# Performance work log

Hardware: AMD Instinct MI355X
Metric: run time of the kernel (lower is better)

The kernel has to match this reference:

```python
import jax, jax.numpy as jnp
import numpy as np

EPS_AGG = 1e-6  # torch code adds 1e-6 to scatter weight sums
EPS_BN = 1e-5


def _pix_idx(loc_orig, H, W):
    # map normalized coords in [-1,1] to flat pixel index on an HxW grid
    loc = jnp.clip(loc_orig, -1.0, 1.0) * 0.5 + 0.5
    ix = jnp.round(loc[..., 0] * (W - 1)).astype(jnp.int32)
    iy = jnp.round(loc[..., 1] * (H - 1)).astype(jnp.int32)
    return iy * W + ix  # [B, N0]


def token2map(x, loc_orig, idx_agg, H, W):
    # scatter token features to a dense map, averaging collisions
    B, N, C = x.shape
    N0 = idx_agg.shape[1]
    idx_hw = _pix_idx(loc_orig, H, W)                                   # [B, N0]
    tok = jnp.take_along_axis(x, idx_agg[..., None], axis=1)            # [B, N0, C]
    flat = (idx_hw + jnp.arange(B, dtype=jnp.int32)[:, None] * (H * W)).reshape(-1)
    sums = jax.ops.segment_sum(tok.reshape(-1, C), flat, num_segments=B * H * W)
    cnt = jax.ops.segment_sum(jnp.ones((B * N0,), x.dtype), flat, num_segments=B * H * W)
    out = sums / (cnt[:, None] + EPS_AGG)
    return out.reshape(B, H, W, C).transpose(0, 3, 1, 2)                # [B, C, H, W]


def map2token(fmap, Nt, loc_orig, idx_agg_t, agg_weight_t):
    # gather map pixels back to Nt target tokens, weighted-averaging per token
    B, C, H, W = fmap.shape
    idx_hw = _pix_idx(loc_orig, H, W)                                   # [B, N0]
    pix = fmap.transpose(0, 2, 3, 1).reshape(B, H * W, C)
    gath = jnp.take_along_axis(pix, idx_hw[..., None], axis=1)          # [B, N0, C]
    flat = (idx_agg_t + jnp.arange(B, dtype=jnp.int32)[:, None] * Nt).reshape(-1)
    num = jax.ops.segment_sum((gath * agg_weight_t[..., None]).reshape(-1, C), flat, num_segments=B * Nt)
    den = jax.ops.segment_sum(agg_weight_t.reshape(-1), flat, num_segments=B * Nt)
    return (num / (den[:, None] + EPS_AGG)).reshape(B, Nt, C)


def token_downup(x, idx_agg_s, idx_agg_t, agg_weight_t, Nt):
    # weighted aggregation from N source tokens to Nt target tokens via N0 original positions
    B, N, C = x.shape
    src = jnp.take_along_axis(x, idx_agg_s[..., None], axis=1)          # [B, N0, C]
    flat = (idx_agg_t + jnp.arange(B, dtype=jnp.int32)[:, None] * Nt).reshape(-1)
    num = jax.ops.segment_sum((src * agg_weight_t[..., None]).reshape(-1, C), flat, num_segments=B * Nt)
    den = jax.ops.segment_sum(agg_weight_t.reshape(-1), flat, num_segments=B * Nt)
    return (num / (den[:, None] + EPS_AGG)).reshape(B, Nt, C)


def batchnorm(x, gamma, beta):
    # BatchNorm2d on [B,C,Nt,1] == per-channel stats over (B, Nt); x here is [B, Nt, C]
    mu = x.mean(axis=(0, 1), keepdims=True)
    var = x.var(axis=(0, 1), keepdims=True)
    return (x - mu) * jax.lax.rsqrt(var + EPS_BN) * gamma + beta


def setup_inputs() -> dict:
    key = jax.random.key(0)
    ks = jax.random.split(key, 12)
    B, N, N0, Nt, Cin, Cout, H, W = 32, 1568, 3136, 784, 256, 512, 56, 56
    x = jax.random.normal(ks[0], (B, N, Cin), dtype=jnp.float32)
    loc_orig = jax.random.uniform(ks[1], (B, N0, 2), dtype=jnp.float32, minval=-1.0, maxval=1.0)
    idx_agg = jax.random.randint(ks[2], (B, N0), 0, N, dtype=jnp.int32)
    agg_weight = jax.random.uniform(ks[3], (B, N0), dtype=jnp.float32)
    idx_agg_t = jax.random.randint(ks[4], (B, N0), 0, Nt, dtype=jnp.int32)
    agg_weight_t = jax.random.uniform(ks[5], (B, N0), dtype=jnp.float32)
    dw_w = jax.random.normal(ks[6], (Cin, 1, 3, 3), dtype=jnp.float32) * 0.1     # depthwise 3x3
    skip_w = jax.random.normal(ks[7], (Cin,), dtype=jnp.float32) * 0.1           # depthwise 1x1
    conv_w = jax.random.normal(ks[8], (Cout, Cin), dtype=jnp.float32) * (1.0 / np.sqrt(Cin))
    gamma1 = jnp.ones((Cin,), jnp.float32); beta1 = jnp.zeros((Cin,), jnp.float32)
    gamma2 = jnp.ones((Cout,), jnp.float32); beta2 = jnp.zeros((Cout,), jnp.float32)
    return {"x": x, "loc_orig": loc_orig, "idx_agg": idx_agg, "agg_weight": agg_weight,
            "idx_agg_t": idx_agg_t, "agg_weight_t": agg_weight_t, "H": H, "W": W, "Nt": Nt,
            "dw_w": dw_w, "skip_w": skip_w, "conv_w": conv_w,
            "gamma1": gamma1, "beta1": beta1, "gamma2": gamma2, "beta2": beta2}


def reference(x, loc_orig, idx_agg, agg_weight, idx_agg_t, agg_weight_t, H, W, Nt,
              dw_w, skip_w, conv_w, gamma1, beta1, gamma2, beta2):
    # token -> map scatter
    x_map = token2map(x, loc_orig, idx_agg, H, W)                       # [B, Cin, H, W]
    # 3x3 depthwise conv, stride 2, padding 1
    Cin = x_map.shape[1]
    x_map = jax.lax.conv_general_dilated(
        x_map, dw_w, window_strides=(2, 2), padding=((1, 1), (1, 1)),
        feature_group_count=Cin, dimension_numbers=("NCHW", "OIHW", "NCHW"))    # [B, Cin, H/2, W/2]
    # map -> target tokens gather
    x_back = map2token(x_map, Nt, loc_orig, idx_agg_t, agg_weight_t)    # [B, Nt, Cin]
    # skip path: token downsample + 1x1 depthwise (per-channel scale)
    xs = token_downup(x, idx_agg, idx_agg_t, agg_weight_t, Nt)          # [B, Nt, Cin]
    xs = xs * skip_w                                                    # dw_skip, groups=Cin, k=1
    y = xs + x_back
    y = batchnorm(y, gamma1, beta1)
    y = jnp.einsum("bnc,oc->bno", y, conv_w)                            # 1x1 conv Cin->Cout
    y = batchnorm(y, gamma2, beta2)
    return jax.nn.relu(y)                                               # [B, Nt, Cout]
```

## Files before the change

kernel.cpp:

```cpp
#include <hip/hip_runtime.h>

constexpr int B    = 32;
constexpr int N    = 1568;
constexpr int N0   = 3136;
constexpr int Nt   = 784;
constexpr int Cin  = 256;
constexpr int Cout = 512;
constexpr int H    = 56;
constexpr int W    = 56;
constexpr int HW   = 3136;
constexpr int Ho   = 28;
constexpr int Wo   = 28;
constexpr int HWo  = 784;
constexpr int RR   = B * Nt;
constexpr int NE   = B * N0;
constexpr int NBP  = B * HW;
constexpr int NBT  = B * Nt;
constexpr int NBO  = B * HWo;
constexpr int SB   = NBT + NBO;
constexpr int NCHUNK = SB / 256;
constexpr int NG   = 32;

constexpr size_t W_HISTP = 0;
constexpr size_t W_HISTS = NBP;
constexpr size_t W_S2SUM = NBP + SB;
constexpr size_t W_S2SQ  = W_S2SUM + Cout;
constexpr size_t W_S1P   = W_S2SQ + Cout;
constexpr size_t W_S1QP  = W_S1P + (size_t)NG * Cin;
constexpr size_t W_MEND  = W_S1QP + (size_t)NG * Cin;
constexpr size_t W_OFF   = W_MEND;
constexpr size_t W_CUR   = W_OFF + SB + 8;
constexpr size_t W_PC    = W_CUR + SB;
constexpr size_t W_BSUM  = W_PC + NE;
constexpr size_t W_LT    = W_BSUM + 512;
constexpr size_t W_LC    = W_LT + (size_t)2 * NE;
constexpr size_t W_CONVB = W_LC + (size_t)8 * NE;
constexpr size_t W_YBF   = W_CONVB + (size_t)B * HWo * Cin / 2;
constexpr size_t W_WFB   = W_YBF + (size_t)RR * Cin / 2;
constexpr size_t W_BIAS  = W_WFB + (size_t)Cout * Cin / 2;
constexpr size_t W_ZB    = W_BIAS + Cout;

__device__ __forceinline__ int pix_of(float t, float scale) {
    t = fminf(fmaxf(t, -1.0f), 1.0f);
    float u = __fadd_rn(__fmul_rn(t, 0.5f), 0.5f);
    return (int)rintf(__fmul_rn(u, scale));
}
__device__ __forceinline__ unsigned short f2bf(float f) {
    unsigned int u = __float_as_uint(f);
    u = (u + 0x7fffu + ((u >> 16) & 1u)) >> 16;
    return (unsigned short)u;
}
__device__ __forceinline__ float bf2f(unsigned short h) {
    return __uint_as_float(((unsigned int)h) << 16);
}
__device__ __forceinline__ void gload_lds16(const void* g, void* lds) {
    __builtin_amdgcn_global_load_lds(
        (const __attribute__((address_space(1))) void*)g,
        (__attribute__((address_space(3))) void*)lds, 16, 0, 0);
}

__global__ void k_hist(const float* __restrict__ loc, const int* __restrict__ idxt,
                       int* __restrict__ histP, int* __restrict__ histS,
                       int* __restrict__ pc) {
    int i = blockIdx.x * 256 + threadIdx.x;
    if (i >= NE) return;
    int b = i / N0;
    float lx = loc[(size_t)2 * i], ly = loc[(size_t)2 * i + 1];
    int ix = pix_of(lx, 55.0f), iy = pix_of(ly, 55.0f);
    int jx = pix_of(lx, 27.0f), jy = pix_of(ly, 27.0f);
    int p56 = iy * W + ix, p28 = jy * Wo + jx;
    pc[i] = p56 | (p28 << 16);
    atomicAdd(&histP[b * HW + p56], 1);
    atomicAdd(&histS[b * Nt + idxt[i]], 1);
    int oy_lo = iy >> 1, oy_hi = min(Ho - 1, (iy + 1) >> 1);
    int ox_lo = ix >> 1, ox_hi = min(Wo - 1, (ix + 1) >> 1);
    for (int oy = oy_lo; oy <= oy_hi; ++oy)
        for (int ox = ox_lo; ox <= ox_hi; ++ox)
            atomicAdd(&histS[NBT + b * HWo + oy * Wo + ox], 1);
}

__global__ void k_scanA(const int* __restrict__ hist, int* __restrict__ bsum) {
    __shared__ int sm[256];
    int i = blockIdx.x * 256 + threadIdx.x;
    sm[threadIdx.x] = hist[i];
    __syncthreads();
    for (int d = 128; d > 0; d >>= 1) {
        if (threadIdx.x < d) sm[threadIdx.x] += sm[threadIdx.x + d];
        __syncthreads();
    }
    if (threadIdx.x == 0) bsum[blockIdx.x] = sm[0];
}

__global__ void k_scanC(const int* __restrict__ hist, const int* __restrict__ bsum,
                        int* __restrict__ off, int* __restrict__ cur) {
    __shared__ int sm[256];
    __shared__ int sb[256];
    int t = threadIdx.x;
    int i = blockIdx.x * 256 + t;
    sb[t] = (t < NCHUNK && t < (int)blockIdx.x) ? bsum[t] : 0;
    int v = hist[i];
    sm[t] = v; __syncthreads();
    for (int d = 128; d > 0; d >>= 1) {
        if (t < d) sb[t] += sb[t + d];
        __syncthreads();
    }
    int base = sb[0];
    __syncthreads();
    for (int d = 1; d < 256; d <<= 1) {
        int u = (t >= d) ? sm[t - d] : 0;
        __syncthreads();
        sm[t] += u;
        __syncthreads();
    }
    int excl = base + sm[t] - v;
    off[i] = excl; cur[i] = excl;
    if (i == SB - 1) off[SB] = excl + v;
}

__global__ void k_scat(const int* __restrict__ pc, const int* __restrict__ idxa,
                       const int* __restrict__ idxt, const float* __restrict__ wt,
                       const int* __restrict__ histP, int* __restrict__ cur,
                       int2* __restrict__ listT, int2* __restrict__ listC) {
    int i = blockIdx.x * 256 + threadIdx.x;
    if (i >= NE) return;
    int b = i / N0;
    int v = pc[i];
    int p56 = v & 0xFFFF, p28 = v >> 16;
    int s = idxa[i];
    int posT = atomicAdd(&cur[b * Nt + idxt[i]], 1);
    listT[posT] = make_int2(s | (p28 << 16), __float_as_int(wt[i]));
    float wrc = 1.0f / ((float)histP[b * HW + p56] + 1e-6f);
    int wrci = __float_as_int(wrc);
    int iy = p56 / W, ix = p56 - iy * W;
    int oy_lo = iy >> 1, oy_hi = min(Ho - 1, (iy + 1) >> 1);
    int ox_lo = ix >> 1, ox_hi = min(Wo - 1, (ix + 1) >> 1);
    for (int oy = oy_lo; oy <= oy_hi; ++oy)
        for (int ox = ox_lo; ox <= ox_hi; ++ox) {
            int tap = (iy - (2 * oy - 1)) * 3 + (ix - (2 * ox - 1));
            int posC = atomicAdd(&cur[NBT + b * HWo + oy * Wo + ox], 1) - NE;
            listC[posC] = make_int2(s | (tap << 16), wrci);
        }
}

__global__ __launch_bounds__(256) void k_gconv(const float* __restrict__ x,
        const int* __restrict__ off, const int2* __restrict__ listC,
        const float* __restrict__ dww, unsigned short* __restrict__ convb) {
    __shared__ float wsm[9 * 256];
    int t = threadIdx.x;
#pragma unroll
    for (int k = 0; k < 9; ++k) wsm[k * 256 + t] = dww[t * 9 + k];
    int wv = t >> 6, lane = t & 63;
    int blk = blockIdx.x * 4 + wv;
    int b   = __builtin_amdgcn_readfirstlane(blk / HWo);
    int st  = __builtin_amdgcn_readfirstlane(off[NBT + blk]) - NE;
    int en  = __builtin_amdgcn_readfirstlane(off[NBT + blk + 1]) - NE;
    __syncthreads();
    const float* xb = x + (size_t)b * N * Cin;
    float4 acc = make_float4(0.f, 0.f, 0.f, 0.f);
    for (int base = st; base < en; base += 64) {
        int n = en - base; if (n > 64) n = 64;
        int2 e = make_int2(0, 0);
        if (lane < n) e = listC[base + lane];
        int j = 0;
        for (; j + 4 <= n; j += 4) {
            int ex0 = __builtin_amdgcn_readlane(e.x, j + 0);
            int ey0 = __builtin_amdgcn_readlane(e.y, j + 0);
            int ex1 = __builtin_amdgcn_readlane(e.x, j + 1);
            int ey1 = __builtin_amdgcn_readlane(e.y, j + 1);
            int ex2 = __builtin_amdgcn_readlane(e.x, j + 2);
            int ey2 = __builtin_amdgcn_readlane(e.y, j + 2);
            int ex3 = __builtin_amdgcn_readlane(e.x, j + 3);
            int ey3 = __builtin_amdgcn_readlane(e.y, j + 3);
            float4 v0 = ((const float4*)(xb + (size_t)(ex0 & 0xFFFF) * Cin))[lane];
            float4 v1 = ((const float4*)(xb + (size_t)(ex1 & 0xFFFF) * Cin))[lane];
            float4 v2 = ((const float4*)(xb + (size_t)(ex2 & 0xFFFF) * Cin))[lane];
            float4 v3 = ((const float4*)(xb + (size_t)(ex3 & 0xFFFF) * Cin))[lane];
            float4 w0 = *(const float4*)&wsm[(ex0 >> 16) * 256 + lane * 4];
            float4 w1 = *(const float4*)&wsm[(ex1 >> 16) * 256 + lane * 4];
            float4 w2 = *(const float4*)&wsm[(ex2 >> 16) * 256 + lane * 4];
            float4 w3 = *(const float4*)&wsm[(ex3 >> 16) * 256 + lane * 4];
            float r0 = __int_as_float(ey0), r1 = __int_as_float(ey1);
            float r2 = __int_as_float(ey2), r3 = __int_as_float(ey3);
            acc.x = fmaf(v0.x * r0, w0.x, acc.x);
            acc.y = fmaf(v0.y * r0, w0.y, acc.y);
            acc.z = fmaf(v0.z * r0, w0.z, acc.z);
            acc.w = fmaf(v0.w * r0, w0.w, acc.w);
            acc.x = fmaf(v1.x * r1, w1.x, acc.x);
            acc.y = fmaf(v1.y * r1, w1.y, acc.y);
            acc.z = fmaf(v1.z * r1, w1.z, acc.z);
            acc.w = fmaf(v1.w * r1, w1.w, acc.w);
            acc.x = fmaf(v2.x * r2, w2.x, acc.x);
            acc.y = fmaf(v2.y * r2, w2.y, acc.y);
            acc.z = fmaf(v2.z * r2, w2.z, acc.z);
            acc.w = fmaf(v2.w * r2, w2.w, acc.w);
            acc.x = fmaf(v3.x * r3, w3.x, acc.x);
            acc.y = fmaf(v3.y * r3, w3.y, acc.y);
            acc.z = fmaf(v3.z * r3, w3.z, acc.z);
            acc.w = fmaf(v3.w * r3, w3.w, acc.w);
        }
        for (; j < n; ++j) {
            int ex = __builtin_amdgcn_readlane(e.x, j);
            int ey = __builtin_amdgcn_readlane(e.y, j);
            float4 v = ((const float4*)(xb + (size_t)(ex & 0xFFFF) * Cin))[lane];
            float4 wq = *(const float4*)&wsm[(ex >> 16) * 256 + lane * 4];
            float r = __int_as_float(ey);
            acc.x = fmaf(v.x * r, wq.x, acc.x);
            acc.y = fmaf(v.y * r, wq.y, acc.y);
            acc.z = fmaf(v.z * r, wq.z, acc.z);
            acc.w = fmaf(v.w * r, wq.w, acc.w);
        }
    }
    uint2 o;
    o.x = (unsigned int)f2bf(acc.x) | ((unsigned int)f2bf(acc.y) << 16);
    o.y = (unsigned int)f2bf(acc.z) | ((unsigned int)f2bf(acc.w) << 16);
    ((uint2*)(convb + (size_t)blk * Cin))[lane] = o;
}

__global__ __launch_bounds__(256) void k_gtok(const float* __restrict__ x,
        const unsigned short* __restrict__ convb, const int* __restrict__ off,
        const int2* __restrict__ listT, const float* __restrict__ skipw,
        unsigned short* __restrict__ ybf, float* __restrict__ s1p,
        float* __restrict__ s1qp) {
    __shared__ float smS[4][256];
    __shared__ float smQ[4][256];
    int t = threadIdx.x, wv = t >> 6, lane = t & 63;
    int bt = blockIdx.x * 4 + wv;
    int b  = __builtin_amdgcn_readfirstlane(bt / Nt);
    int st = __builtin_amdgcn_readfirstlane(off[bt]);
    int en = __builtin_amdgcn_readfirstlane(off[bt + 1]);
    const float* xb = x + (size_t)b * N * Cin;
    const unsigned short* cbb = convb + (size_t)b * HWo * Cin;
    float4 sk = ((const float4*)skipw)[lane];
    float4 acc = make_float4(0.f, 0.f, 0.f, 0.f);
    float wsum = 0.0f;
    for (int base = st; base < en; base += 64) {
        int n = en - base; if (n > 64) n = 64;
        int2 e = make_int2(0, 0);
        if (lane < n) e = listT[base + lane];
        int j = 0;
        for (; j + 2 <= n; j += 2) {
            int ex0 = __builtin_amdgcn_readlane(e.x, j + 0);
            int ey0 = __builtin_amdgcn_readlane(e.y, j + 0);
            int ex1 = __builtin_amdgcn_readlane(e.x, j + 1);
            int ey1 = __builtin_amdgcn_readlane(e.y, j + 1);
            float4 xv0 = ((const float4*)(xb + (size_t)(ex0 & 0xFFFF) * Cin))[lane];
            float4 xv1 = ((const float4*)(xb + (size_t)(ex1 & 0xFFFF) * Cin))[lane];
            uint2 cv0 = ((const uint2*)(cbb + (size_t)(ex0 >> 16) * Cin))[lane];
            uint2 cv1 = ((const uint2*)(cbb + (size_t)(ex1 >> 16) * Cin))[lane];
            float w0 = __int_as_float(ey0), w1 = __int_as_float(ey1);
            wsum += w0 + w1;
            acc.x = fmaf(w0, bf2f((unsigned short)(cv0.x & 0xffffu)) + sk.x * xv0.x, acc.x);
            acc.y = fmaf(w0, bf2f((unsigned short)(cv0.x >> 16))     + sk.y * xv0.y, acc.y);
            acc.z = fmaf(w0, bf2f((unsigned short)(cv0.y & 0xffffu)) + sk.z * xv0.z, acc.z);
            acc.w = fmaf(w0, bf2f((unsigned short)(cv0.y >> 16))     + sk.w * xv0.w, acc.w);
            acc.x = fmaf(w1, bf2f((unsigned short)(cv1.x & 0xffffu)) + sk.x * xv1.x, acc.x);
            acc.y = fmaf(w1, bf2f((unsigned short)(cv1.x >> 16))     + sk.y * xv1.y, acc.y);
            acc.z = fmaf(w1, bf2f((unsigned short)(cv1.y & 0xffffu)) + sk.z * xv1.z, acc.z);
            acc.w = fmaf(w1, bf2f((unsigned short)(cv1.y >> 16))     + sk.w * xv1.w, acc.w);
        }
        for (; j < n; ++j) {
            int ex = __builtin_amdgcn_readlane(e.x, j);
            int ey = __builtin_amdgcn_readlane(e.y, j);
            float4 xv = ((const float4*)(xb + (size_t)(ex & 0xFFFF) * Cin))[lane];
            uint2 cv = ((const uint2*)(cbb + (size_t)(ex >> 16) * Cin))[lane];
            float w = __int_as_float(ey);
            wsum += w;
            acc.x = fmaf(w, bf2f((unsigned short)(cv.x & 0xffffu)) + sk.x * xv.x, acc.x);
            acc.y = fmaf(w, bf2f((unsigned short)(cv.x >> 16))     + sk.y * xv.y, acc.y);
            acc.z = fmaf(w, bf2f((unsigned short)(cv.y & 0xffffu)) + sk.z * xv.z, acc.z);
            acc.w = fmaf(w, bf2f((unsigned short)(cv.y >> 16))     + sk.w * xv.w, acc.w);
        }
    }
    float rw = 1.0f / (wsum + 1e-6f);
    float y0 = acc.x * rw, y1 = acc.y * rw, y2 = acc.z * rw, y3 = acc.w * rw;
    smS[wv][lane * 4 + 0] = y0; smQ[wv][lane * 4 + 0] = y0 * y0;
    smS[wv][lane * 4 + 1] = y1; smQ[wv][lane * 4 + 1] = y1 * y1;
    smS[wv][lane * 4 + 2] = y2; smQ[wv][lane * 4 + 2] = y2 * y2;
    smS[wv][lane * 4 + 3] = y3; smQ[wv][lane * 4 + 3] = y3 * y3;
    uint2 o;
    o.x = (unsigned int)f2bf(y0) | ((unsigned int)f2bf(y1) << 16);
    o.y = (unsigned int)f2bf(y2) | ((unsigned int)f2bf(y3) << 16);
    ((uint2*)(ybf + (size_t)bt * Cin))[lane] = o;
    __syncthreads();
    float ps = smS[0][t] + smS[1][t] + smS[2][t] + smS[3][t];
    float pq = smQ[0][t] + smQ[1][t] + smQ[2][t] + smQ[3][t];
    int g = (blockIdx.x & (NG - 1)) * Cin + t;
    atomicAdd(&s1p[g],  ps);
    atomicAdd(&s1qp[g], pq);
}

__global__ void k_fold(const float* __restrict__ s1p, const float* __restrict__ s1qp,
                       const float* __restrict__ g1, const float* __restrict__ b1,
                       const float* __restrict__ convw, unsigned short* __restrict__ wfb,
                       float* __restrict__ bias) {
    int o = blockIdx.x, c = threadIdx.x;
    const float inv = 1.0f / (float)RR;
    float s = 0.0f, q = 0.0f;
#pragma unroll
    for (int g = 0; g < NG; ++g) { s += s1p[g * Cin + c]; q += s1qp[g * Cin + c]; }
    float mu  = s * inv;
    float var = q * inv - mu * mu;
    float a   = g1[c] / sqrtf(var + 1e-5f);
    float bs  = b1[c] - mu * a;
    float wv  = convw[(size_t)o * Cin + c];
    wfb[(size_t)o * Cin + c] = f2bf(wv * a);
    __shared__ float red[256];
    red[c] = wv * bs;
    __syncthreads();
    for (int st = 128; st > 0; st >>= 1) {
        if (c < st) red[c] += red[c + st];
        __syncthreads();
    }
    if (c == 0) bias[o] = red[0];
}

typedef __attribute__((ext_vector_type(8))) short short8;
typedef __attribute__((ext_vector_type(4))) float f32x4;

__global__ __launch_bounds__(256, 4) void k_gemm(const unsigned short* __restrict__ A,
        const unsigned short* __restrict__ Bt, const float* __restrict__ bias,
        unsigned short* __restrict__ zb, float* __restrict__ s2, float* __restrict__ s2q) {
    __shared__ unsigned short As[2][128 * 32];
    __shared__ unsigned short Bs[2][128 * 32];
    __shared__ float rsum[128], rsq[128];
    int m0 = blockIdx.x * 128, n0 = blockIdx.y * 128;
    int t = threadIdx.x;
    int wave = t >> 6, lane = t & 63;
    int wm = wave >> 1, wn = wave & 1;
    int l16 = lane & 15, lq = lane >> 4;
    if (t < 128) { rsum[t] = 0.0f; rsq[t] = 0.0f; }

    int r_off = lane >> 2;
    int sc    = (lane & 3) ^ ((lane >> 4) & 3);
    const unsigned short* Asrc = A  + (size_t)(m0 + r_off) * Cin + sc * 8;
    const unsigned short* Bsrc = Bt + (size_t)(n0 + r_off) * Cin + sc * 8;
    int r0a = wave * 32, r0b = r0a + 16;

    auto STAGE = [&](int buf, int k0) {
        gload_lds16(Asrc + (size_t)r0a * Cin + k0, &As[buf][r0a * 32]);
        gload_lds16(Asrc + (size_t)r0b * Cin + k0, &As[buf][r0b * 32]);
        gload_lds16(Bsrc + (size_t)r0a * Cin + k0, &Bs[buf][r0a * 32]);
        gload_lds16(Bsrc + (size_t)r0b * Cin + k0, &Bs[buf][r0b * 32]);
    };

    int ckoff = (lq ^ ((l16 >> 2) & 3)) * 8;
    int rbA = (wm * 64 + l16) * 32 + ckoff;
    int rbB = (wn * 64 + l16) * 32 + ckoff;

    f32x4 acc[4][4];
#pragma unroll
    for (int i = 0; i < 4; ++i)
#pragma unroll
        for (int j = 0; j < 4; ++j) acc[i][j] = (f32x4)0.0f;

    STAGE(0, 0);
    __syncthreads();
#pragma unroll
    for (int ks = 0; ks < 8; ++ks) {
        int cur = ks & 1;
        if (ks < 7) STAGE(cur ^ 1, (ks + 1) * 32);
        short8 af[4], bf[4];
#pragma unroll
        for (int i = 0; i < 4; ++i) af[i] = *(short8*)&As[cur][rbA + i * 512];
#pragma unroll
        for (int j = 0; j < 4; ++j) bf[j] = *(short8*)&Bs[cur][rbB + j * 512];
#pragma unroll
        for (int i = 0; i < 4; ++i)
#pragma unroll
            for (int j = 0; j < 4; ++j)
                acc[i][j] = __builtin_amdgcn_mfma_f32_16x16x32_bf16(af[i], bf[j], acc[i][j], 0, 0, 0);
        __syncthreads();
    }

#pragma unroll
    for (int j = 0; j < 4; ++j) {
        int cl  = wn * 64 + j * 16 + l16;
        int col = n0 + cl;
        float bv = bias[col];
        float ps = 0.0f, pq = 0.0f;
#pragma unroll
        for (int i = 0; i < 4; ++i) {
            int rbase = m0 + wm * 64 + i * 16 + lq * 4;
#pragma unroll
            for (int r = 0; r < 4; ++r) {
                float v = acc[i][j][r] + bv;
                zb[(size_t)(rbase + r) * Cout + col] = f2bf(v);
                ps += v;
                pq = fmaf(v, v, pq);
            }
        }
        atomicAdd(&rsum[cl], ps);
        atomicAdd(&rsq[cl], pq);
    }
    __syncthreads();
    if (t < 128) {
        atomicAdd(&s2[n0 + t], rsum[t]);
        atomicAdd(&s2q[n0 + t], rsq[t]);
    }
}

__global__ void k_final(const unsigned short* __restrict__ zb,
                        const float* __restrict__ s2, const float* __restrict__ s2q,
                        const float* __restrict__ g2, const float* __restrict__ b2,
                        float* __restrict__ out) {
    size_t j4 = ((size_t)blockIdx.x * 256 + threadIdx.x) * 4;
    int o = (int)(j4 & (Cout - 1));
    const float inv = 1.0f / (float)RR;
    uint2 u = *(const uint2*)&zb[j4];
    float e0 = bf2f((unsigned short)(u.x & 0xffffu));
    float e1 = bf2f((unsigned short)(u.x >> 16));
    float e2 = bf2f((unsigned short)(u.y & 0xffffu));
    float e3 = bf2f((unsigned short)(u.y >> 16));
    float mu0 = s2[o + 0] * inv, a0 = g2[o + 0] * rsqrtf(s2q[o + 0] * inv - mu0 * mu0 + 1e-5f);
    float mu1 = s2[o + 1] * inv, a1 = g2[o + 1] * rsqrtf(s2q[o + 1] * inv - mu1 * mu1 + 1e-5f);
    float mu2 = s2[o + 2] * inv, a2 = g2[o + 2] * rsqrtf(s2q[o + 2] * inv - mu2 * mu2 + 1e-5f);
    float mu3 = s2[o + 3] * inv, a3 = g2[o + 3] * rsqrtf(s2q[o + 3] * inv - mu3 * mu3 + 1e-5f);
    float c0 = b2[o + 0] - mu0 * a0;
    float c1 = b2[o + 1] - mu1 * a1;
    float c2 = b2[o + 2] - mu2 * a2;
    float c3 = b2[o + 3] - mu3 * a3;
    float4 r;
    r.x = fmaxf(fmaf(e0, a0, c0), 0.0f);
    r.y = fmaxf(fmaf(e1, a1, c1), 0.0f);
    r.z = fmaxf(fmaf(e2, a2, c2), 0.0f);
    r.w = fmaxf(fmaf(e3, a3, c3), 0.0f);
    *(float4*)&out[j4] = r;
}

extern "C" void kernel_launch(void* const* d_in, const int* in_sizes, int n_in,
                              void* d_out, int out_size, void* d_ws, size_t ws_size,
                              hipStream_t stream) {
    const float* x     = (const float*)d_in[0];
    const float* loc   = (const float*)d_in[1];
    const int*   idxa  = (const int*)d_in[2];
    const int*   idxt  = (const int*)d_in[4];
    const float* wt    = (const float*)d_in[5];
    const float* dww   = (const float*)d_in[9];
    const float* skipw = (const float*)d_in[10];
    const float* convw = (const float*)d_in[11];
    const float* g1    = (const float*)d_in[12];
    const float* b1    = (const float*)d_in[13];
    const float* g2    = (const float*)d_in[14];
    const float* b2    = (const float*)d_in[15];

    float* ws = (float*)d_ws;
    int*   histP = (int*)(ws + W_HISTP);
    int*   histS = (int*)(ws + W_HISTS);
    float* s2sum = ws + W_S2SUM;
    float* s2sq  = ws + W_S2SQ;
    float* s1p   = ws + W_S1P;
    float* s1qp  = ws + W_S1QP;
    int*   off   = (int*)(ws + W_OFF);
    int*   cur   = (int*)(ws + W_CUR);
    int*   pc    = (int*)(ws + W_PC);
    int*   bsum  = (int*)(ws + W_BSUM);
    int2*  listT = (int2*)(ws + W_LT);
    int2*  listC = (int2*)(ws + W_LC);
    unsigned short* convb = (unsigned short*)(ws + W_CONVB);
    unsigned short* ybf   = (unsigned short*)(ws + W_YBF);
    unsigned short* wfb   = (unsigned short*)(ws + W_WFB);
    float* bias  = ws + W_BIAS;
    unsigned short* zb = (unsigned short*)(ws + W_ZB);
    float* out   = (float*)d_out;

    hipMemsetAsync(histP, 0, (size_t)W_MEND * sizeof(float), stream);

    k_hist<<<NE / 256, 256, 0, stream>>>(loc, idxt, histP, histS, pc);
    k_scanA<<<NCHUNK, 256, 0, stream>>>(histS, bsum);
    k_scanC<<<NCHUNK, 256, 0, stream>>>(histS, bsum, off, cur);
    k_scat<<<NE / 256, 256, 0, stream>>>(pc, idxa, idxt, wt, histP, cur, listT, listC);

    k_gconv<<<NBO / 4, 256, 0, stream>>>(x, off, listC, dww, convb);
    k_gtok<<<NBT / 4, 256, 0, stream>>>(x, convb, off, listT, skipw, ybf, s1p, s1qp);
    k_fold<<<Cout, 256, 0, stream>>>(s1p, s1qp, g1, b1, convw, wfb, bias);

    dim3 gg(RR / 128, Cout / 128);
    k_gemm<<<gg, 256, 0, stream>>>(ybf, wfb, bias, zb, s2sum, s2sq);
    k_final<<<(int)(((size_t)RR * Cout) / 1024), 256, 0, stream>>>(zb, s2sum, s2sq, g2, b2, out);
}
```

Measured before the change: 248.8 us.

## Fuse final batchnorm and ReLU into GEMM via cooperative grid sync

Moves the second batchnorm and ReLU into a cooperative-launched GEMM kernel. Accumulators stay in registers across a grid-wide sync that waits for the global column statistics, then the kernel writes the normalized output directly. This removes the bf16 intermediate write and read of the GEMM result and the separate final kernel launch. In exchange it needs all 784 blocks resident at once, adds a grid barrier and keeps registers live across it. If the cooperative launch fails, the old two-kernel path runs instead.

```diff
diff --git a/kernel.cpp b/kernel.cpp
--- a/kernel.cpp
+++ b/kernel.cpp
@@ -1,4 +1,6 @@
 #include <hip/hip_runtime.h>
+#include <hip/hip_cooperative_groups.h>
+namespace cg = cooperative_groups;
 
 constexpr int B    = 32;
 constexpr int N    = 1568;
@@ -317,12 +319,11 @@
 typedef __attribute__((ext_vector_type(8))) short short8;
 typedef __attribute__((ext_vector_type(4))) float f32x4;
 
-__global__ __launch_bounds__(256, 4) void k_gemm(const unsigned short* __restrict__ A,
-        const unsigned short* __restrict__ Bt, const float* __restrict__ bias,
-        unsigned short* __restrict__ zb, float* __restrict__ s2, float* __restrict__ s2q) {
-    __shared__ unsigned short As[2][128 * 32];
-    __shared__ unsigned short Bs[2][128 * 32];
-    __shared__ float rsum[128], rsq[128];
+template <typename EPI>
+__device__ __forceinline__ void gemm_body(const unsigned short* A,
+        const unsigned short* Bt, const float* bias, float* s2, float* s2q,
+        unsigned short* As_, unsigned short* Bs_, float* rsum, float* rsq,
+        f32x4 (&acc)[4][4], EPI&& epi_store) {
     int m0 = blockIdx.x * 128, n0 = blockIdx.y * 128;
     int t = threadIdx.x;
     int wave = t >> 6, lane = t & 63;
@@ -337,17 +338,16 @@
     int r0a = wave * 32, r0b = r0a + 16;
 
     auto STAGE = [&](int buf, int k0) {
-        gload_lds16(Asrc + (size_t)r0a * Cin + k0, &As[buf][r0a * 32]);
-        gload_lds16(Asrc + (size_t)r0b * Cin + k0, &As[buf][r0b * 32]);
-        gload_lds16(Bsrc + (size_t)r0a * Cin + k0, &Bs[buf][r0a * 32]);
-        gload_lds16(Bsrc + (size_t)r0b * Cin + k0, &Bs[buf][r0b * 32]);
+        gload_lds16(Asrc + (size_t)r0a * Cin + k0, &As_[buf * 128 * 32 + r0a * 32]);
+        gload_lds16(Asrc + (size_t)r0b * Cin + k0, &As_[buf * 128 * 32 + r0b * 32]);
+        gload_lds16(Bsrc + (size_t)r0a * Cin + k0, &Bs_[buf * 128 * 32 + r0a * 32]);
+        gload_lds16(Bsrc + (size_t)r0b * Cin + k0, &Bs_[buf * 128 * 32 + r0b * 32]);
     };
 
     int ckoff = (lq ^ ((l16 >> 2) & 3)) * 8;
     int rbA = (wm * 64 + l16) * 32 + ckoff;
     int rbB = (wn * 64 + l16) * 32 + ckoff;
 
-    f32x4 acc[4][4];
 #pragma unroll
     for (int i = 0; i < 4; ++i)
 #pragma unroll
@@ -361,9 +361,9 @@
         if (ks < 7) STAGE(cur ^ 1, (ks + 1) * 32);
         short8 af[4], bf[4];
 #pragma unroll
-        for (int i = 0; i < 4; ++i) af[i] = *(short8*)&As[cur][rbA + i * 512];
-#pragma unroll
-        for (int j = 0; j < 4; ++j) bf[j] = *(short8*)&Bs[cur][rbB + j * 512];
+        for (int i = 0; i < 4; ++i) af[i] = *(short8*)&As_[cur * 128 * 32 + rbA + i * 512];
+#pragma unroll
+        for (int j = 0; j < 4; ++j) bf[j] = *(short8*)&Bs_[cur * 128 * 32 + rbB + j * 512];
 #pragma unroll
         for (int i = 0; i < 4; ++i)
 #pragma unroll
@@ -384,7 +384,8 @@
 #pragma unroll
             for (int r = 0; r < 4; ++r) {
                 float v = acc[i][j][r] + bv;
-                zb[(size_t)(rbase + r) * Cout + col] = f2bf(v);
+                acc[i][j][r] = v;
+                epi_store(rbase + r, col, v);
                 ps += v;
                 pq = fmaf(v, v, pq);
             }
@@ -396,6 +397,55 @@
     if (t < 128) {
         atomicAdd(&s2[n0 + t], rsum[t]);
         atomicAdd(&s2q[n0 + t], rsq[t]);
+    }
+}
+
+__global__ __launch_bounds__(256, 4) void k_gemm(const unsigned short* __restrict__ A,
+        const unsigned short* __restrict__ Bt, const float* __restrict__ bias,
+        unsigned short* __restrict__ zb, float* __restrict__ s2, float* __restrict__ s2q) {
+    __shared__ unsigned short As[2 * 128 * 32];
+    __shared__ unsigned short Bs[2 * 128 * 32];
+    __shared__ float rsum[128], rsq[128];
+    f32x4 acc[4][4];
+    gemm_body(A, Bt, bias, s2, s2q, As, Bs, rsum, rsq, acc,
+              [&](int row, int col, float v) {
+                  zb[(size_t)row * Cout + col] = f2bf(v);
+              });
+}
+
+__global__ __launch_bounds__(256, 4) void k_gemm_coop(const unsigned short* __restrict__ A,
+        const unsigned short* __restrict__ Bt, const float* __restrict__ bias,
+        float* __restrict__ s2, float* __restrict__ s2q,
+        const float* __restrict__ g2, const float* __restrict__ b2,
+        float* __restrict__ out) {
+    __shared__ unsigned short As[2 * 128 * 32];
+    __shared__ unsigned short Bs[2 * 128 * 32];
+    __shared__ float rsum[128], rsq[128];
+    f32x4 acc[4][4];
+    gemm_body(A, Bt, bias, s2, s2q, As, Bs, rsum, rsq, acc,
+              [](int, int, float) {});
+    cg::this_grid().sync();
+
+    int m0 = blockIdx.x * 128, n0 = blockIdx.y * 128;
+    int t = threadIdx.x;
+    int wave = t >> 6, lane = t & 63;
+    int wm = wave >> 1, wn = wave & 1;
+    int l16 = lane & 15, lq = lane >> 4;
+    const float inv = 1.0f / (float)RR;
+#pragma unroll
+    for (int j = 0; j < 4; ++j) {
+        int col = n0 + wn * 64 + j * 16 + l16;
+        float mu = s2[col] * inv;
+        float a  = g2[col] * rsqrtf(s2q[col] * inv - mu * mu + 1e-5f);
+        float c  = b2[col] - mu * a;
+#pragma unroll
+        for (int i = 0; i < 4; ++i) {
+            int rbase = m0 + wm * 64 + i * 16 + lq * 4;
+#pragma unroll
+            for (int r = 0; r < 4; ++r)
+                out[(size_t)(rbase + r) * Cout + col] =
+                    fmaxf(fmaf(acc[i][j][r], a, c), 0.0f);
+        }
     }
 }
 
@@ -475,6 +525,19 @@
     k_fold<<<Cout, 256, 0, stream>>>(s1p, s1qp, g1, b1, convw, wfb, bias);
 
     dim3 gg(RR / 128, Cout / 128);
-    k_gemm<<<gg, 256, 0, stream>>>(ybf, wfb, bias, zb, s2sum, s2sq);
-    k_final<<<(int)(((size_t)RR * Cout) / 1024), 256, 0, stream>>>(zb, s2sum, s2sq, g2, b2, out);
-}
+    {
+        const unsigned short* A = ybf;
+        const unsigned short* Bt = wfb;
+        const float* biasc = bias;
+        void* args[] = {(void*)&A, (void*)&Bt, (void*)&biasc,
+                        (void*)&s2sum, (void*)&s2sq,
+                        (void*)&g2, (void*)&b2, (void*)&out};
+        hipError_t err = hipLaunchCooperativeKernel((const void*)k_gemm_coop,
+                                                    gg, dim3(256), args, 0, stream);
+        if (err != hipSuccess) {
+            k_gemm<<<gg, 256, 0, stream>>>(ybf, wfb, bias, zb, s2sum, s2sq);
+            k_final<<<(int)(((size_t)RR * Cout) / 1024), 256, 0, stream>>>(
+                zb, s2sum, s2sq, g2, b2, out);
+        }
+    }
+}
```

Result: slower. 360.5 us (+44.9%).
